# Kernel tuning notes

Hardware: AMD Instinct MI355X
Metric: run time of the kernel (lower is better)

Reference implementation:

```python
import jax, jax.numpy as jnp
import numpy as np


def setup_inputs() -> dict:
    key = jax.random.key(0)
    k1, k2 = jax.random.split(key)
    B, T, D = 32, 512, 256
    x = jax.random.normal(k1, (B, T, D), dtype=jnp.float32)
    x_pred_dur = jax.random.randint(k2, (B, T), 0, 8, dtype=jnp.int32)
    return {"x": x, "x_pred_dur": x_pred_dur, "max_dur": 4096}


def reference(x, x_pred_dur, max_dur):
    # x: [B, T, D] float phoneme features; x_pred_dur: [B, T] int frame counts.
    # Equivalent to repeat_interleave along T per batch, padded to max_dur.
    B, T, D = x.shape
    cum = jnp.cumsum(x_pred_dur, axis=1)              # [B, T] exclusive-end offsets
    total = cum[:, -1]                                # [B] mel lengths
    frames = jnp.arange(max_dur, dtype=cum.dtype)     # [M]
    # For each output frame j, the source phoneme is the first t with cum[t] > j.
    idx = jax.vmap(lambda c: jnp.searchsorted(c, frames, side='right'))(cum)  # [B, M]
    idx = jnp.minimum(idx, T - 1)                     # clamp out-of-range (padding region)
    out = jnp.take_along_axis(x, idx[..., None], axis=1)     # [B, M, D] gather
    valid = (frames[None, :] < total[:, None])[..., None]    # [B, M, 1]
    out = jnp.where(valid, out, jnp.zeros((), dtype=x.dtype))
    return out, total.astype(jnp.int32)
```

## Files before the change

### kernel.cpp

```cpp
#include <hip/hip_runtime.h>

#define BB 32
#define TT 512
#define DD 256
#define MAXDUR 4096
#define D4 (DD / 4)
#define FPB 64

__global__ __launch_bounds__(256)
void lr_fused_kernel(const float* __restrict__ x,
                     const int* __restrict__ dur,
                     float* __restrict__ out,
                     float* __restrict__ out_total) {
    __shared__ int scum[TT];
    __shared__ int sp[256];
    __shared__ int sidx[FPB];

    const int blocksPerBatch = MAXDUR / FPB;
    const int b = blockIdx.x / blocksPerBatch;
    const int chunk = blockIdx.x % blocksPerBatch;
    const int f0 = chunk * FPB;
    const int tid = threadIdx.x;

    int2 d2 = ((const int2*)(dur + b * TT))[tid];
    const int a0 = d2.x;
    const int a1 = d2.x + d2.y;
    sp[tid] = a1;
    __syncthreads();
    #pragma unroll
    for (int off = 1; off < 256; off <<= 1) {
        int v = (tid >= off) ? sp[tid - off] : 0;
        __syncthreads();
        sp[tid] += v;
        __syncthreads();
    }
    const int off_excl = sp[tid] - a1;
    scum[2 * tid]     = off_excl + a0;
    scum[2 * tid + 1] = off_excl + a1;
    __syncthreads();

    const int total = scum[TT - 1];
    if (chunk == 0 && tid == 0) {
        out_total[b] = (float)total;
    }

    if (tid < FPB) {
        const int f = f0 + tid;
        int lo = 0, hi = TT;
        #pragma unroll
        for (int it = 0; it < 9; ++it) {
            int mid = (lo + hi) >> 1;
            if (lo < hi) {
                if (scum[mid] <= f) lo = mid + 1; else hi = mid;
            }
        }
        int idx = lo < TT - 1 ? lo : TT - 1;
        sidx[tid] = (f < total) ? idx : -1;
    }
    __syncthreads();

    const int vec = tid & 63;
    const int fl  = tid >> 6;
    const float4* __restrict__ x4 = (const float4*)x;
    float4* __restrict__ out4 = (float4*)out;
    const float4 zero = make_float4(0.f, 0.f, 0.f, 0.f);

    #pragma unroll
    for (int it = 0; it < FPB / 4; ++it) {
        const int flocal = it * 4 + fl;
        const int f = f0 + flocal;
        const int idx = sidx[flocal];
        float4 v = zero;
        if (idx >= 0) {
            v = x4[((size_t)b * TT + idx) * D4 + vec];
        }
        out4[((size_t)b * MAXDUR + f) * D4 + vec] = v;
    }
}

extern "C" void kernel_launch(void* const* d_in, const int* in_sizes, int n_in,
                              void* d_out, int out_size, void* d_ws, size_t ws_size,
                              hipStream_t stream) {
    const float* x   = (const float*)d_in[0];
    const int*   dur = (const int*)d_in[1];

    float* out = (float*)d_out;
    float* out_total = out + (size_t)BB * MAXDUR * DD;

    lr_fused_kernel<<<BB * (MAXDUR / FPB), 256, 0, stream>>>(x, dur, out, out_total);
}
```

Measured before the change: 28.12 us.

## Replace shared-memory scan and search with per-wave shuffle scan

Each wave now computes the prefix sum of durations itself. Every lane sums 8 durations serially, then a wavefront shuffle scan combines them, and a shuffle-based binary search finds the source row for each frame. This removes the block-wide LDS Hillis-Steele scan with its many __syncthreads barriers, along with the shared index table. The cost is that all 4 waves redundantly do the scan and search, and the copy loop pays extra shuffle instructions.

```diff
diff --git a/kernel.cpp b/kernel.cpp
--- a/kernel.cpp
+++ b/kernel.cpp
@@ -12,69 +12,80 @@
                      const int* __restrict__ dur,
                      float* __restrict__ out,
                      float* __restrict__ out_total) {
-    __shared__ int scum[TT];
-    __shared__ int sp[256];
-    __shared__ int sidx[FPB];
-
     const int blocksPerBatch = MAXDUR / FPB;
     const int b = blockIdx.x / blocksPerBatch;
     const int chunk = blockIdx.x % blocksPerBatch;
     const int f0 = chunk * FPB;
     const int tid = threadIdx.x;
+    const int lane = tid & 63;
+    const int wid = tid >> 6;
 
-    int2 d2 = ((const int2*)(dur + b * TT))[tid];
-    const int a0 = d2.x;
-    const int a1 = d2.x + d2.y;
-    sp[tid] = a1;
-    __syncthreads();
+    const int4* dp = (const int4*)(dur + b * TT + lane * 8);
+    const int4 da = dp[0];
+    const int4 db_ = dp[1];
+
+    int s0 = da.x;
+    int s1 = s0 + da.y;
+    int s2 = s1 + da.z;
+    int s3 = s2 + da.w;
+    int s4 = s3 + db_.x;
+    int s5 = s4 + db_.y;
+    int s6 = s5 + db_.z;
+    int s7 = s6 + db_.w;
+    const int lt = s7;
+
+    int incl = lt;
     #pragma unroll
-    for (int off = 1; off < 256; off <<= 1) {
-        int v = (tid >= off) ? sp[tid - off] : 0;
-        __syncthreads();
-        sp[tid] += v;
-        __syncthreads();
+    for (int off = 1; off < 64; off <<= 1) {
+        int v = __shfl_up(incl, off, 64);
+        if (lane >= off) incl += v;
     }
-    const int off_excl = sp[tid] - a1;
-    scum[2 * tid]     = off_excl + a0;
-    scum[2 * tid + 1] = off_excl + a1;
-    __syncthreads();
+    const int excl = incl - lt;
+    s0 += excl; s1 += excl; s2 += excl; s3 += excl;
+    s4 += excl; s5 += excl; s6 += excl; s7 += excl;
 
-    const int total = scum[TT - 1];
+    const int total = __shfl(incl, 63, 64);
     if (chunk == 0 && tid == 0) {
         out_total[b] = (float)total;
     }
 
-    if (tid < FPB) {
-        const int f = f0 + tid;
-        int lo = 0, hi = TT;
-        #pragma unroll
-        for (int it = 0; it < 9; ++it) {
-            int mid = (lo + hi) >> 1;
-            if (lo < hi) {
-                if (scum[mid] <= f) lo = mid + 1; else hi = mid;
-            }
-        }
-        int idx = lo < TT - 1 ? lo : TT - 1;
-        sidx[tid] = (f < total) ? idx : -1;
+    const int F = f0 + lane;
+    int pos = 0;
+    #pragma unroll
+    for (int st = 32; st >= 1; st >>= 1) {
+        const int cand = pos + st;
+        const int v = __shfl(incl, cand - 1, 64);
+        if (v <= F) pos = cand;
     }
-    __syncthreads();
+    const int psel = pos < 64 ? pos : 63;
+    const int v0 = __shfl(s0, psel, 64);
+    const int v1 = __shfl(s1, psel, 64);
+    const int v2 = __shfl(s2, psel, 64);
+    const int v3 = __shfl(s3, psel, 64);
+    const int v4 = __shfl(s4, psel, 64);
+    const int v5 = __shfl(s5, psel, 64);
+    const int v6 = __shfl(s6, psel, 64);
+    const int v7 = __shfl(s7, psel, 64);
+    const int inner = (v0 <= F) + (v1 <= F) + (v2 <= F) + (v3 <= F) +
+                      (v4 <= F) + (v5 <= F) + (v6 <= F) + (v7 <= F);
+    const int U = psel * 8 + inner;
+    const int row = U < TT - 1 ? U : TT - 1;
+    const int rowOrNeg = (F < total) ? row : -1;
 
-    const int vec = tid & 63;
-    const int fl  = tid >> 6;
     const float4* __restrict__ x4 = (const float4*)x;
     float4* __restrict__ out4 = (float4*)out;
     const float4 zero = make_float4(0.f, 0.f, 0.f, 0.f);
 
     #pragma unroll
     for (int it = 0; it < FPB / 4; ++it) {
-        const int flocal = it * 4 + fl;
+        const int flocal = it * 4 + wid;
+        const int ridx = __shfl(rowOrNeg, flocal, 64);
         const int f = f0 + flocal;
-        const int idx = sidx[flocal];
         float4 v = zero;
-        if (idx >= 0) {
-            v = x4[((size_t)b * TT + idx) * D4 + vec];
+        if (ridx >= 0) {
+            v = x4[((size_t)b * TT + ridx) * D4 + lane];
         }
-        out4[((size_t)b * MAXDUR + f) * D4 + vec] = v;
+        out4[((size_t)b * MAXDUR + f) * D4 + lane] = v;
     }
 }
 
```

New measurement: 27.55 us. -2.0%, faster.
